# Kernel optimization log

Hardware: AMD Instinct MI355X
Metric: run time of the kernel (lower is better)

## Reference

```python
import jax, jax.numpy as jnp
import numpy as np

H = 1024   # hidden_size
B = 4096   # batch
C = 2      # num_classes

def setup_inputs() -> dict:
    key = jax.random.key(0)
    ks = jax.random.split(key, 12)
    s = 0.02
    return {
        "h": jax.random.normal(ks[0], (2, B, H), jnp.float32),
        "c": jax.random.normal(ks[1], (2, B, H), jnp.float32),
        # torch nn.LSTM params: W_ih_l0 (4H, C), W_hh_l0 (4H, H), biases (4H,)
        "W_ih0": jax.random.normal(ks[2], (4 * H, C), jnp.float32) * s,
        "W_hh0": jax.random.normal(ks[3], (4 * H, H), jnp.float32) * s,
        "b_ih0": jax.random.normal(ks[4], (4 * H,), jnp.float32) * s,
        "b_hh0": jax.random.normal(ks[5], (4 * H,), jnp.float32) * s,
        "W_ih1": jax.random.normal(ks[6], (4 * H, H), jnp.float32) * s,
        "W_hh1": jax.random.normal(ks[7], (4 * H, H), jnp.float32) * s,
        "b_ih1": jax.random.normal(ks[8], (4 * H,), jnp.float32) * s,
        "b_hh1": jax.random.normal(ks[9], (4 * H,), jnp.float32) * s,
        "fc_W": jax.random.normal(ks[10], (C, H), jnp.float32) * s,
        "fc_b": jax.random.normal(ks[11], (C,), jnp.float32) * s,
        "pred_len": 64,
    }

def _lstm_cell(gates, c_prev):
    # torch gate order: input, forget, cell(g), output
    i, f, g, o = jnp.split(gates, 4, axis=1)
    c_new = jax.nn.sigmoid(f) * c_prev + jax.nn.sigmoid(i) * jnp.tanh(g)
    h_new = jax.nn.sigmoid(o) * jnp.tanh(c_new)
    return h_new, c_new

def reference(h, c, W_ih0, W_hh0, b_ih0, b_hh0, W_ih1, W_hh1, b_ih1, b_hh1, fc_W, fc_b, pred_len):
    h0, h1 = h[0], h[1]
    c0, c1 = c[0], c[1]
    x0 = jnp.zeros((h0.shape[0], fc_W.shape[0]), h.dtype)  # (B, C)

    def step(carry, _):
        h0, c0, h1, c1, x = carry
        g0 = x @ W_ih0.T + b_ih0 + h0 @ W_hh0.T + b_hh0
        h0n, c0n = _lstm_cell(g0, c0)
        g1 = h0n @ W_ih1.T + b_ih1 + h1 @ W_hh1.T + b_hh1
        h1n, c1n = _lstm_cell(g1, c1)
        logit = h1n @ fc_W.T + fc_b                       # (B, C)
        # greedy argmax feedback (targets=None branch)
        x_next = jax.nn.one_hot(jnp.argmax(logit, axis=1), logit.shape[1], dtype=logit.dtype)
        return (h0n, c0n, h1n, c1n, x_next), logit

    _, logits = jax.lax.scan(step, (h0, c0, h1, c1, x0), None, length=pred_len)
    return jnp.transpose(logits, (1, 0, 2))  # (B, pred_len, C)
```

## Files before the change

### kernel.cpp

```cpp
#include <hip/hip_runtime.h>
#include <stdint.h>

#define H_ 1024
#define NG_ 4096

typedef float f32x4 __attribute__((ext_vector_type(4)));
typedef __bf16 bf16x8 __attribute__((ext_vector_type(8)));

__device__ __forceinline__ unsigned short f2bf(float f) {
  union { float f; uint32_t u; } v; v.f = f;
  uint32_t r = v.u + 0x7FFFu + ((v.u >> 16) & 1u);
  return (unsigned short)(r >> 16);
}
__device__ __forceinline__ float bf2f(unsigned short b) {
  union { uint32_t u; float f; } v; v.u = ((uint32_t)b) << 16; return v.f;
}

__device__ __forceinline__ void gload_lds16(const void* g, void* l) {
  __builtin_amdgcn_global_load_lds(
      (const __attribute__((address_space(1))) void*)g,
      (__attribute__((address_space(3))) void*)l, 16, 0, 0);
}

__device__ __forceinline__ float sigm(float x) { return 1.f / (1.f + __expf(-x)); }
__device__ __forceinline__ float tanh_(float x) { return 1.f - 2.f / (__expf(2.f * x) + 1.f); }

__global__ void prep_w0(const float* __restrict__ Whh0, unsigned short* __restrict__ Wr) {
  int i = (blockIdx.x * 256 + threadIdx.x) * 4;
  int r = i >> 10, k = i & 1023;
  int gate = (r >> 4) & 3;
  int j = ((r >> 6) << 4) + (r & 15);
  const float4 v = *(const float4*)(Whh0 + (size_t)(gate * H_ + j) * H_ + k);
  ushort4 o; o.x = f2bf(v.x); o.y = f2bf(v.y); o.z = f2bf(v.z); o.w = f2bf(v.w);
  *(ushort4*)(Wr + i) = o;
}

__global__ void prep_wcat(const float* __restrict__ Wih1, const float* __restrict__ Whh1,
                          unsigned short* __restrict__ Wr) {
  int i = (blockIdx.x * 256 + threadIdx.x) * 4;
  int r = i >> 11, k = i & 2047;
  int gate = (r >> 4) & 3;
  int j = ((r >> 6) << 4) + (r & 15);
  const float* src = (k < 1024) ? (Wih1 + (size_t)(gate * H_ + j) * H_ + k)
                                : (Whh1 + (size_t)(gate * H_ + j) * H_ + (k - 1024));
  const float4 v = *(const float4*)src;
  ushort4 o; o.x = f2bf(v.x); o.y = f2bf(v.y); o.z = f2bf(v.z); o.w = f2bf(v.w);
  *(ushort4*)(Wr + (size_t)r * 2048 + k) = o;
}

__global__ void prep_small(const float* __restrict__ Wih0,
                           const float* __restrict__ bih0, const float* __restrict__ bhh0,
                           const float* __restrict__ bih1, const float* __restrict__ bhh1,
                           float* __restrict__ bias0r, float* __restrict__ bias1r,
                           float* __restrict__ wi0r) {
  int r = blockIdx.x * 256 + threadIdx.x;
  int gate = (r >> 4) & 3;
  int j = ((r >> 6) << 4) + (r & 15);
  int old = gate * H_ + j;
  bias0r[r] = bih0[old] + bhh0[old];
  bias1r[r] = bih1[old] + bhh1[old];
  wi0r[r * 2 + 0] = Wih0[old * 2 + 0];
  wi0r[r * 2 + 1] = Wih0[old * 2 + 1];
}

__global__ void prep_state(const float* __restrict__ h, const float* __restrict__ c,
                           unsigned short* __restrict__ h0b, unsigned short* __restrict__ h1b,
                           float* __restrict__ c0, float* __restrict__ c1, int bh) {
  int i = (blockIdx.x * 256 + threadIdx.x) * 4;
  float4 a = *(const float4*)(h + i);
  float4 b = *(const float4*)(h + (size_t)bh + i);
  ushort4 oa; oa.x = f2bf(a.x); oa.y = f2bf(a.y); oa.z = f2bf(a.z); oa.w = f2bf(a.w);
  ushort4 ob; ob.x = f2bf(b.x); ob.y = f2bf(b.y); ob.z = f2bf(b.z); ob.w = f2bf(b.w);
  *(ushort4*)(h0b + i) = oa;
  *(ushort4*)(h1b + i) = ob;
  *(float4*)(c0 + i) = *(const float4*)(c + i);
  *(float4*)(c1 + i) = *(const float4*)(c + (size_t)bh + i);
}

__global__ void __launch_bounds__(256, 4)
lstm_gemm_cell(const unsigned short* __restrict__ A0,
               const unsigned short* __restrict__ A1,
               int Ktot,
               const unsigned short* __restrict__ Bw,
               const float* __restrict__ biasr,
               const float* __restrict__ wi0r,
               const float* __restrict__ xlog,
               float* __restrict__ Cst,
               unsigned short* __restrict__ Hout,
               const float* __restrict__ fcW,
               const float* __restrict__ fcb,
               float* __restrict__ outT,
               int pl2) {
  __shared__ unsigned short As[128 * 64];
  __shared__ unsigned short Bs[128 * 64];
  const int tid  = threadIdx.x;
  const int lane = tid & 63;
  const int wv   = tid >> 6;
  const int wm   = wv >> 1, wn = wv & 1;

  const int wgid = blockIdx.y * 32 + blockIdx.x;
  const int swz  = ((wgid & 7) << 7) | (wgid >> 3);
  const int tile_m = (swz >> 5) * 128;
  const int tile_n = (swz & 31) * 128;

  f32x4 acc[4][4];
#pragma unroll
  for (int m = 0; m < 4; ++m)
#pragma unroll
    for (int n = 0; n < 4; ++n) acc[m][n] = (f32x4)0.f;

  const int lrow = lane >> 3;
  const int lk   = ((lane & 7) ^ lrow) * 8;

  const int nk = Ktot >> 6;
  for (int kt = 0; kt < nk; ++kt) {
    const int k0 = kt << 6;
    const unsigned short* Ap; int kl;
    if (k0 < 1024) { Ap = A0; kl = k0; } else { Ap = A1; kl = k0 - 1024; }
#pragma unroll
    for (int i = 0; i < 4; ++i) {
      int chunk = wv * 4 + i;
      int row = chunk * 8 + lrow;
      gload_lds16(Ap + (size_t)(tile_m + row) * H_ + kl + lk, (void*)&As[chunk * 512]);
    }
#pragma unroll
    for (int i = 0; i < 4; ++i) {
      int chunk = wv * 4 + i;
      int row = chunk * 8 + lrow;
      gload_lds16(Bw + (size_t)(tile_n + row) * Ktot + k0 + lk, (void*)&Bs[chunk * 512]);
    }
    __syncthreads();

    const char* Ab = (const char*)As;
    const char* Bb = (const char*)Bs;
    const int arow = wm * 64 + (lane & 15);
    const int brow = wn * 64 + (lane & 15);
    const int khi  = lane >> 4;
    const int x7   = lane & 7;
    const int ksw0 = ((0 + khi) ^ x7) * 16;
    const int ksw1 = ((4 + khi) ^ x7) * 16;
#pragma unroll
    for (int ks = 0; ks < 2; ++ks) {
      const int ksw = ks ? ksw1 : ksw0;
      bf16x8 af[4], bfr[4];
#pragma unroll
      for (int m = 0; m < 4; ++m)
        af[m] = *(const bf16x8*)(Ab + (arow + m * 16) * 128 + ksw);
#pragma unroll
      for (int n = 0; n < 4; ++n)
        bfr[n] = *(const bf16x8*)(Bb + (brow + n * 16) * 128 + ksw);
#pragma unroll
      for (int m = 0; m < 4; ++m)
#pragma unroll
        for (int n = 0; n < 4; ++n)
          acc[m][n] = __builtin_amdgcn_mfma_f32_16x16x32_bf16(af[m], bfr[n], acc[m][n], 0, 0, 0);
    }
    __syncthreads();
  }

  const int cl = lane & 15;
  const int rq = (lane >> 4) * 4;
  const int jgrp = (tile_n >> 6) + wn;
  const int j = jgrp * 16 + cl;
  float bias[4], w0v[4] = {0, 0, 0, 0}, w1v[4] = {0, 0, 0, 0};
  const int have_x = (xlog != nullptr);
#pragma unroll
  for (int n = 0; n < 4; ++n) {
    int colr = tile_n + wn * 64 + n * 16 + cl;
    bias[n] = biasr[colr];
    if (have_x) { w0v[n] = wi0r[colr * 2]; w1v[n] = wi0r[colr * 2 + 1]; }
  }
  float fW0 = 0.f, fW1 = 0.f;
  if (fcW) { fW0 = fcW[j]; fW1 = fcW[H_ + j]; }
  const int add_bias = (tile_n == 0) && (wn == 0);

#pragma unroll
  for (int m = 0; m < 4; ++m) {
#pragma unroll
    for (int q = 0; q < 4; ++q) {
      int row = tile_m + wm * 64 + m * 16 + rq + q;
      float gi = acc[m][0][q] + bias[0];
      float gf = acc[m][1][q] + bias[1];
      float gg = acc[m][2][q] + bias[2];
      float go = acc[m][3][q] + bias[3];
      if (have_x) {
        const float* xr = xlog + (size_t)row * pl2;
        int x = xr[1] > xr[0];
        gi += x ? w1v[0] : w0v[0];
        gf += x ? w1v[1] : w0v[1];
        gg += x ? w1v[2] : w0v[2];
        go += x ? w1v[3] : w0v[3];
      }
      size_t off = (size_t)row * H_ + j;
      float cp = Cst[off];
      float cn = sigm(gf) * cp + sigm(gi) * tanh_(gg);
      float hn = sigm(go) * tanh_(cn);
      Cst[off] = cn;
      Hout[off] = f2bf(hn);
      if (fcW) {
        float d0 = hn * fW0, d1 = hn * fW1;
#pragma unroll
        for (int s = 1; s < 16; s <<= 1) {
          d0 += __shfl_xor(d0, s);
          d1 += __shfl_xor(d1, s);
        }
        if (cl == 0) {
          if (add_bias) { d0 += fcb[0]; d1 += fcb[1]; }
          float* op = outT + (size_t)row * pl2;
          atomicAdd(op, d0);
          atomicAdd(op + 1, d1);
        }
      }
    }
  }
}

extern "C" void kernel_launch(void* const* d_in, const int* in_sizes, int n_in,
                              void* d_out, int out_size, void* d_ws, size_t ws_size,
                              hipStream_t stream) {
  const float* h     = (const float*)d_in[0];
  const float* c     = (const float*)d_in[1];
  const float* Wih0  = (const float*)d_in[2];
  const float* Whh0  = (const float*)d_in[3];
  const float* bih0  = (const float*)d_in[4];
  const float* bhh0  = (const float*)d_in[5];
  const float* Wih1  = (const float*)d_in[6];
  const float* Whh1  = (const float*)d_in[7];
  const float* bih1  = (const float*)d_in[8];
  const float* bhh1  = (const float*)d_in[9];
  const float* fcW   = (const float*)d_in[10];
  const float* fcb   = (const float*)d_in[11];

  const int B = in_sizes[0] / (2 * H_);
  const int pred_len = out_size / (B * 2);
  const int BH = B * H_;
  const int pl2 = pred_len * 2;

  size_t off = 0;
  auto carve = [&](size_t bytes) -> void* {
    void* p = (char*)d_ws + off;
    off += (bytes + 255) & ~(size_t)255;
    return p;
  };
  unsigned short* Whh0r = (unsigned short*)carve((size_t)NG_ * 1024 * 2);
  unsigned short* Wcatr = (unsigned short*)carve((size_t)NG_ * 2048 * 2);
  unsigned short* h0b[2], *h1b[2];
  h0b[0] = (unsigned short*)carve((size_t)BH * 2);
  h0b[1] = (unsigned short*)carve((size_t)BH * 2);
  h1b[0] = (unsigned short*)carve((size_t)BH * 2);
  h1b[1] = (unsigned short*)carve((size_t)BH * 2);
  float* c0 = (float*)carve((size_t)BH * 4);
  float* c1 = (float*)carve((size_t)BH * 4);
  float* bias0r = (float*)carve(NG_ * 4);
  float* bias1r = (float*)carve(NG_ * 4);
  float* wi0r   = (float*)carve(NG_ * 2 * 4);

  hipMemsetAsync(d_out, 0, (size_t)out_size * sizeof(float), stream);

  hipLaunchKernelGGL(prep_w0,   dim3((NG_ * 1024 / 4) / 256), dim3(256), 0, stream, Whh0, Whh0r);
  hipLaunchKernelGGL(prep_wcat, dim3((NG_ * 2048 / 4) / 256), dim3(256), 0, stream, Wih1, Whh1, Wcatr);
  hipLaunchKernelGGL(prep_small, dim3(NG_ / 256), dim3(256), 0, stream,
                     Wih0, bih0, bhh0, bih1, bhh1, bias0r, bias1r, wi0r);
  hipLaunchKernelGGL(prep_state, dim3((BH / 4) / 256), dim3(256), 0, stream,
                     h, c, h0b[0], h1b[0], c0, c1, BH);

  dim3 ggrid(NG_ / 128, B / 128);
  dim3 gblk(256);
  float* out = (float*)d_out;

  for (int t = 0; t < pred_len; ++t) {
    const int cur = t & 1, nxt = cur ^ 1;
    hipLaunchKernelGGL(lstm_gemm_cell, ggrid, gblk, 0, stream,
                       h0b[cur], (const unsigned short*)nullptr, 1024, Whh0r,
                       bias0r, wi0r,
                       (t > 0) ? (out + (size_t)(t - 1) * 2) : (const float*)nullptr,
                       c0, h0b[nxt],
                       (const float*)nullptr, (const float*)nullptr, (float*)nullptr, pl2);
    hipLaunchKernelGGL(lstm_gemm_cell, ggrid, gblk, 0, stream,
                       h0b[nxt], h1b[cur], 2048, Wcatr,
                       bias1r, (const float*)nullptr,
                       (const float*)nullptr,
                       c1, h1b[nxt],
                       fcW, fcb, out + (size_t)t * 2, pl2);
  }
}
```

Before: 8.648 ms.

## Replace FC atomics with partial-sum buffer reduced in next step's kernel

The layer-1 kernel writes per-column-group FC partial dot products into a scratch buffer instead of issuing global atomicAdds into the output. The next step's layer-0 kernel reduces these partials per row, writes the logits, and computes the argmax flag into shared memory, and a final kernel handles the last step. The memset is dropped and the workgroup tile swizzle is removed. Each layer-0 block now redundantly re-reduces 128 partials for its rows, and removing the swizzle may change L2 locality.

Measured after the change: 7.677 ms. 11.2% less time.

```diff
diff --git a/kernel.cpp b/kernel.cpp
--- a/kernel.cpp
+++ b/kernel.cpp
@@ -84,24 +84,39 @@
                const unsigned short* __restrict__ Bw,
                const float* __restrict__ biasr,
                const float* __restrict__ wi0r,
-               const float* __restrict__ xlog,
+               const float* __restrict__ fcpart_in,
+               const float* __restrict__ fcb,
+               float* __restrict__ outPrev,
+               int pl2,
                float* __restrict__ Cst,
                unsigned short* __restrict__ Hout,
                const float* __restrict__ fcW,
-               const float* __restrict__ fcb,
-               float* __restrict__ outT,
-               int pl2) {
+               float* __restrict__ fcpart_out) {
   __shared__ unsigned short As[128 * 64];
   __shared__ unsigned short Bs[128 * 64];
+  __shared__ unsigned char xflag[128];
   const int tid  = threadIdx.x;
   const int lane = tid & 63;
   const int wv   = tid >> 6;
   const int wm   = wv >> 1, wn = wv & 1;
-
-  const int wgid = blockIdx.y * 32 + blockIdx.x;
-  const int swz  = ((wgid & 7) << 7) | (wgid >> 3);
-  const int tile_m = (swz >> 5) * 128;
-  const int tile_n = (swz & 31) * 128;
+  const int tile_m = blockIdx.y * 128;
+  const int tile_n = blockIdx.x * 128;
+
+  const int have_x = (fcpart_in != nullptr);
+  if (have_x && tid < 128) {
+    const int row = tile_m + tid;
+    const float* fp = fcpart_in + (size_t)row * 128;
+    float s0 = 0.f, s1 = 0.f;
+#pragma unroll
+    for (int i2 = 0; i2 < 32; ++i2) {
+      float4 v = *(const float4*)(fp + i2 * 4);
+      s0 += v.x + v.z; s1 += v.y + v.w;
+    }
+    s0 += fcb[0]; s1 += fcb[1];
+    outPrev[(size_t)row * pl2 + 0] = s0;
+    outPrev[(size_t)row * pl2 + 1] = s1;
+    xflag[tid] = (s1 > s0) ? 1 : 0;
+  }
 
   f32x4 acc[4][4];
 #pragma unroll
@@ -163,7 +178,6 @@
   const int jgrp = (tile_n >> 6) + wn;
   const int j = jgrp * 16 + cl;
   float bias[4], w0v[4] = {0, 0, 0, 0}, w1v[4] = {0, 0, 0, 0};
-  const int have_x = (xlog != nullptr);
 #pragma unroll
   for (int n = 0; n < 4; ++n) {
     int colr = tile_n + wn * 64 + n * 16 + cl;
@@ -172,7 +186,6 @@
   }
   float fW0 = 0.f, fW1 = 0.f;
   if (fcW) { fW0 = fcW[j]; fW1 = fcW[H_ + j]; }
-  const int add_bias = (tile_n == 0) && (wn == 0);
 
 #pragma unroll
   for (int m = 0; m < 4; ++m) {
@@ -184,8 +197,7 @@
       float gg = acc[m][2][q] + bias[2];
       float go = acc[m][3][q] + bias[3];
       if (have_x) {
-        const float* xr = xlog + (size_t)row * pl2;
-        int x = xr[1] > xr[0];
+        int x = xflag[row - tile_m];
         gi += x ? w1v[0] : w0v[0];
         gf += x ? w1v[1] : w0v[1];
         gg += x ? w1v[2] : w0v[2];
@@ -205,14 +217,26 @@
           d1 += __shfl_xor(d1, s);
         }
         if (cl == 0) {
-          if (add_bias) { d0 += fcb[0]; d1 += fcb[1]; }
-          float* op = outT + (size_t)row * pl2;
-          atomicAdd(op, d0);
-          atomicAdd(op + 1, d1);
+          float2 p; p.x = d0; p.y = d1;
+          *(float2*)(fcpart_out + (size_t)row * 128 + jgrp * 2) = p;
         }
       }
     }
   }
+}
+
+__global__ void fc_finalize(const float* __restrict__ fcpart, const float* __restrict__ fcb,
+                            float* __restrict__ outLast, int pl2) {
+  const int row = blockIdx.x * 256 + threadIdx.x;
+  const float* fp = fcpart + (size_t)row * 128;
+  float s0 = 0.f, s1 = 0.f;
+#pragma unroll
+  for (int i2 = 0; i2 < 32; ++i2) {
+    float4 v = *(const float4*)(fp + i2 * 4);
+    s0 += v.x + v.z; s1 += v.y + v.w;
+  }
+  outLast[(size_t)row * pl2 + 0] = s0 + fcb[0];
+  outLast[(size_t)row * pl2 + 1] = s1 + fcb[1];
 }
 
 extern "C" void kernel_launch(void* const* d_in, const int* in_sizes, int n_in,
@@ -254,8 +278,7 @@
   float* bias0r = (float*)carve(NG_ * 4);
   float* bias1r = (float*)carve(NG_ * 4);
   float* wi0r   = (float*)carve(NG_ * 2 * 4);
-
-  hipMemsetAsync(d_out, 0, (size_t)out_size * sizeof(float), stream);
+  float* fcpart = (float*)carve((size_t)B * 128 * 4);
 
   hipLaunchKernelGGL(prep_w0,   dim3((NG_ * 1024 / 4) / 256), dim3(256), 0, stream, Whh0, Whh0r);
   hipLaunchKernelGGL(prep_wcat, dim3((NG_ * 2048 / 4) / 256), dim3(256), 0, stream, Wih1, Whh1, Wcatr);
@@ -273,14 +296,20 @@
     hipLaunchKernelGGL(lstm_gemm_cell, ggrid, gblk, 0, stream,
                        h0b[cur], (const unsigned short*)nullptr, 1024, Whh0r,
                        bias0r, wi0r,
-                       (t > 0) ? (out + (size_t)(t - 1) * 2) : (const float*)nullptr,
+                       (t > 0) ? (const float*)fcpart : (const float*)nullptr,
+                       fcb,
+                       (t > 0) ? (out + (size_t)(t - 1) * 2) : (float*)nullptr,
+                       pl2,
                        c0, h0b[nxt],
-                       (const float*)nullptr, (const float*)nullptr, (float*)nullptr, pl2);
+                       (const float*)nullptr, (float*)nullptr);
     hipLaunchKernelGGL(lstm_gemm_cell, ggrid, gblk, 0, stream,
                        h0b[nxt], h1b[cur], 2048, Wcatr,
                        bias1r, (const float*)nullptr,
-                       (const float*)nullptr,
+                       (const float*)nullptr, (const float*)nullptr,
+                       (float*)nullptr, pl2,
                        c1, h1b[nxt],
-                       fcW, fcb, out + (size_t)t * 2, pl2);
-  }
-}
+                       fcW, fcpart);
+  }
+  hipLaunchKernelGGL(fc_finalize, dim3(B / 256), dim3(256), 0, stream,
+                     fcpart, fcb, out + (size_t)(pred_len - 1) * 2, pl2);
+}
```
